# Performance work log

Hardware: AMD Instinct MI355X
Metric: run time of the kernel (lower is better)

## Reference

```python
import jax, jax.numpy as jnp
import numpy as np

N = 50000   # nodes
E = 800000  # edges (avg degree 16)
H = 8       # num_heads
D = 16      # head_dim = hidden_size // num_heads = 128 // 8


def setup_inputs() -> dict:
    key = jax.random.key(0)
    k1, k2, k3, k4, k5 = jax.random.split(key, 5)
    q = jax.random.normal(k1, (N, D, H), dtype=jnp.float32)
    k = jax.random.normal(k2, (N, D, H), dtype=jnp.float32)
    v = jax.random.normal(k3, (N, D, H), dtype=jnp.float32)
    # COO adjacency: row = destination node of each edge, col = source node
    row = jnp.sort(jax.random.randint(k4, (E,), 0, N, dtype=jnp.int32))
    col = jax.random.randint(k5, (E,), 0, N, dtype=jnp.int32)
    return {"q": q, "k": k, "v": v, "row": row, "col": col}


def reference(q, k, v, row, col):
    # bsddmm: sampled dense-dense matmul -> per-edge, per-head attention logits
    # logits[e, h] = sum_d q[row[e], d, h] * k[col[e], d, h]
    logits = jnp.einsum('edh,edh->eh', q[row], k[col])  # [E, H]

    # sparse softmax over each destination row (per head), numerically stable
    m = jax.ops.segment_max(logits, row, num_segments=N)  # [N, H]
    p = jnp.exp(logits - m[row])                          # [E, H]
    s = jax.ops.segment_sum(p, row, num_segments=N)       # [N, H]
    attn = p / s[row]                                     # [E, H]

    # bspmm: out[i, d, h] = sum_{e: row[e]==i} attn[e, h] * v[col[e], d, h]
    out = jax.ops.segment_sum(attn[:, None, :] * v[col], row, num_segments=N)  # [N, D, H]
    return out.reshape(N, -1)  # [N, D*H]
```

## Files before the change

kernel.cpp:

```cpp
#include <hip/hip_runtime.h>
#include <math.h>

#define HEADS 8
#define DIM 16
#define NPB 32

static __device__ __forceinline__ unsigned short f2bf(float f) {
  unsigned u = __float_as_uint(f);
  u += 0x7FFFu + ((u >> 16) & 1u);
  return (unsigned short)(u >> 16);
}
static __device__ __forceinline__ float bflo(unsigned u) { return __uint_as_float(u << 16); }
static __device__ __forceinline__ float bfhi(unsigned u) { return __uint_as_float(u & 0xFFFF0000u); }

__global__ __launch_bounds__(256) void conv_kernel(
    const float* __restrict__ k, const float* __restrict__ v,
    unsigned short* __restrict__ kv, int N) {
  int j = blockIdx.x * blockDim.x + threadIdx.x;
  if (j >= N * 32) return;
  int i = j >> 5, c = j & 31;
  const float* src = (c < 16 ? k : v) + (size_t)i * 128 + (c & 15) * 8;
  float4 f0 = ((const float4*)src)[0];
  float4 f1 = ((const float4*)src)[1];
  uint4 r;
  r.x = (unsigned)f2bf(f0.x) | ((unsigned)f2bf(f0.y) << 16);
  r.y = (unsigned)f2bf(f0.z) | ((unsigned)f2bf(f0.w) << 16);
  r.z = (unsigned)f2bf(f1.x) | ((unsigned)f2bf(f1.y) << 16);
  r.w = (unsigned)f2bf(f1.z) | ((unsigned)f2bf(f1.w) << 16);
  *(uint4*)(kv + (size_t)i * 256 + c * 8) = r;
}

__global__ __launch_bounds__(256) void spmha_bf16_kernel(
    const float* __restrict__ q, const unsigned short* __restrict__ kv,
    const int* __restrict__ row, const int* __restrict__ col,
    float* __restrict__ out, int N, int E) {
  __shared__ int rp[NPB + 1];
  int node0 = blockIdx.x * NPB;
  if (threadIdx.x <= NPB) {
    int target = node0 + threadIdx.x;
    int lo = 0, hi = E;
    while (lo < hi) {
      int mid = (lo + hi) >> 1;
      if (row[mid] < target) lo = mid + 1; else hi = mid;
    }
    rp[threadIdx.x] = lo;
  }
  __syncthreads();

  int il = threadIdx.x >> 3;
  int i  = node0 + il;
  int l  = threadIdx.x & 7;
  bool alive = (i < N);
  int s = alive ? rp[il] : 0;
  int e = alive ? rp[il + 1] : 0;

  float qv0[8], qv1[8];
  if (alive) {
    const float4* qp = (const float4*)(q + (size_t)i * 128);
    *(float4*)&qv0[0] = qp[2 * l];
    *(float4*)&qv0[4] = qp[2 * l + 1];
    *(float4*)&qv1[0] = qp[16 + 2 * l];
    *(float4*)&qv1[4] = qp[16 + 2 * l + 1];
  }

  float o0[8], o1[8], m[8], den[8];
#pragma unroll
  for (int h = 0; h < 8; ++h) { o0[h] = 0.f; o1[h] = 0.f; m[h] = -INFINITY; den[h] = 0.f; }

  auto cvt8 = [](const uint4& A, float* f) {
    f[0] = bflo(A.x); f[1] = bfhi(A.x); f[2] = bflo(A.y); f[3] = bfhi(A.y);
    f[4] = bflo(A.z); f[5] = bfhi(A.z); f[6] = bflo(A.w); f[7] = bfhi(A.w);
  };

  auto do_edge = [&](const uint4& A, const uint4& B, const uint4& C, const uint4& D) {
    float kf0[8], kf1[8], vf0[8], vf1[8];
    cvt8(A, kf0); cvt8(B, kf1); cvt8(C, vf0); cvt8(D, vf1);
    float part[8];
#pragma unroll
    for (int h = 0; h < 8; ++h) part[h] = fmaf(qv0[h], kf0[h], qv1[h] * kf1[h]);
#pragma unroll
    for (int h = 0; h < 8; ++h) part[h] += __shfl_xor(part[h], 1);
#pragma unroll
    for (int h = 0; h < 8; ++h) part[h] += __shfl_xor(part[h], 2);
#pragma unroll
    for (int h = 0; h < 8; ++h) part[h] += __shfl_xor(part[h], 4);
#pragma unroll
    for (int h = 0; h < 8; ++h) {
      float mn = fmaxf(m[h], part[h]);
      float sc = __expf(m[h] - mn);
      float p  = __expf(part[h] - mn);
      den[h] = fmaf(den[h], sc, p);
      m[h] = mn;
      o0[h] = fmaf(o0[h], sc, p * vf0[h]);
      o1[h] = fmaf(o1[h], sc, p * vf1[h]);
    }
  };

  int eidx = s;
  for (; eidx + 2 <= e; eidx += 2) {
    int c0 = col[eidx];
    int c1 = col[eidx + 1];
    const uint4* b0 = (const uint4*)(kv + (size_t)c0 * 256);
    const uint4* b1 = (const uint4*)(kv + (size_t)c1 * 256);
    uint4 A0 = b0[l], B0 = b0[8 + l], C0 = b0[16 + l], D0 = b0[24 + l];
    uint4 A1 = b1[l], B1 = b1[8 + l], C1 = b1[16 + l], D1 = b1[24 + l];
    do_edge(A0, B0, C0, D0);
    do_edge(A1, B1, C1, D1);
  }
  if (eidx < e) {
    int c0 = col[eidx];
    const uint4* b0 = (const uint4*)(kv + (size_t)c0 * 256);
    do_edge(b0[l], b0[8 + l], b0[16 + l], b0[24 + l]);
  }

  if (alive) {
    float inv[8];
#pragma unroll
    for (int h = 0; h < 8; ++h) inv[h] = (e > s) ? 1.f / den[h] : 0.f;
    float4* op = (float4*)(out + (size_t)i * 128);
    float4 r;
    r.x = o0[0] * inv[0]; r.y = o0[1] * inv[1]; r.z = o0[2] * inv[2]; r.w = o0[3] * inv[3];
    op[2 * l] = r;
    r.x = o0[4] * inv[4]; r.y = o0[5] * inv[5]; r.z = o0[6] * inv[6]; r.w = o0[7] * inv[7];
    op[2 * l + 1] = r;
    r.x = o1[0] * inv[0]; r.y = o1[1] * inv[1]; r.z = o1[2] * inv[2]; r.w = o1[3] * inv[3];
    op[16 + 2 * l] = r;
    r.x = o1[4] * inv[4]; r.y = o1[5] * inv[5]; r.z = o1[6] * inv[6]; r.w = o1[7] * inv[7];
    op[16 + 2 * l + 1] = r;
  }
}

__global__ __launch_bounds__(256) void spmha_f32_kernel(
    const float* __restrict__ q, const float* __restrict__ k, const float* __restrict__ v,
    const int* __restrict__ row, const int* __restrict__ col,
    float* __restrict__ out, int N, int E) {
  __shared__ int rp[NPB + 1];
  int node0 = blockIdx.x * NPB;
  if (threadIdx.x <= NPB) {
    int target = node0 + threadIdx.x;
    int lo = 0, hi = E;
    while (lo < hi) {
      int mid = (lo + hi) >> 1;
      if (row[mid] < target) lo = mid + 1; else hi = mid;
    }
    rp[threadIdx.x] = lo;
  }
  __syncthreads();

  int il = threadIdx.x >> 3;
  int i  = node0 + il;
  int l  = threadIdx.x & 7;
  bool alive = (i < N);
  int s = alive ? rp[il] : 0;
  int e = alive ? rp[il + 1] : 0;

  float qv[16];
  if (alive) {
    const float4* qb = (const float4*)(q + (size_t)i * 128);
#pragma unroll
    for (int r = 0; r < 4; ++r) *(float4*)&qv[4 * r] = qb[8 * r + l];
  }
  float o[16];
#pragma unroll
  for (int x = 0; x < 16; ++x) o[x] = 0.f;
  float m[4], den[4];
#pragma unroll
  for (int j = 0; j < 4; ++j) { m[j] = -INFINITY; den[j] = 0.f; }

  auto do_edge = [&](const float* kk, const float* vv) {
    float part[4];
#pragma unroll
    for (int j = 0; j < 4; ++j) part[j] = 0.f;
#pragma unroll
    for (int r = 0; r < 4; ++r)
#pragma unroll
      for (int j = 0; j < 4; ++j)
        part[j] = fmaf(qv[4 * r + j], kk[4 * r + j], part[j]);
#pragma unroll
    for (int j = 0; j < 4; ++j) {
      part[j] += __shfl_xor(part[j], 2);
      part[j] += __shfl_xor(part[j], 4);
    }
#pragma unroll
    for (int j = 0; j < 4; ++j) {
      float mn = fmaxf(m[j], part[j]);
      float sc = __expf(m[j] - mn);
      float p  = __expf(part[j] - mn);
      den[j] = fmaf(den[j], sc, p);
      m[j] = mn;
#pragma unroll
      for (int r = 0; r < 4; ++r)
        o[4 * r + j] = fmaf(o[4 * r + j], sc, p * vv[4 * r + j]);
    }
  };

  int eidx = s;
  for (; eidx < e; ++eidx) {
    int c0 = col[eidx];
    const float4* kb0 = (const float4*)(k + (size_t)c0 * 128);
    const float4* vb0 = (const float4*)(v + (size_t)c0 * 128);
    float kk0[16], vv0[16];
#pragma unroll
    for (int r = 0; r < 4; ++r) {
      *(float4*)&kk0[4 * r] = kb0[8 * r + l];
      *(float4*)&vv0[4 * r] = vb0[8 * r + l];
    }
    do_edge(kk0, vv0);
  }

  if (alive) {
    float inv[4];
#pragma unroll
    for (int j = 0; j < 4; ++j) inv[j] = (e > s) ? 1.f / den[j] : 0.f;
    float4* ob = (float4*)(out + (size_t)i * 128);
#pragma unroll
    for (int r = 0; r < 4; ++r) {
      float4 res;
      res.x = o[4 * r + 0] * inv[0];
      res.y = o[4 * r + 1] * inv[1];
      res.z = o[4 * r + 2] * inv[2];
      res.w = o[4 * r + 3] * inv[3];
      ob[8 * r + l] = res;
    }
  }
}

extern "C" void kernel_launch(void* const* d_in, const int* in_sizes, int n_in,
                              void* d_out, int out_size, void* d_ws, size_t ws_size,
                              hipStream_t stream) {
  const float* q   = (const float*)d_in[0];
  const float* k   = (const float*)d_in[1];
  const float* v   = (const float*)d_in[2];
  const int*   row = (const int*)d_in[3];
  const int*   col = (const int*)d_in[4];
  float* out = (float*)d_out;

  int N = in_sizes[0] / (DIM * HEADS);
  int E = in_sizes[3];

  size_t kv_bytes = (size_t)N * 512;
  int total = N * HEADS;
  int grid = (total + 255) / 256;

  if (ws_size >= kv_bytes) {
    unsigned short* kv = (unsigned short*)d_ws;
    int cgrid = (N * 32 + 255) / 256;
    conv_kernel<<<cgrid, 256, 0, stream>>>(k, v, kv, N);
    spmha_bf16_kernel<<<grid, 256, 0, stream>>>(q, kv, row, col, out, N, E);
  } else {
    spmha_f32_kernel<<<grid, 256, 0, stream>>>(q, k, v, row, col, out, N, E);
  }
}
```

Baseline: 239.8 us.

## Split each node's edge list across two thread groups and merge softmax states

The bf16 kernel now assigns two 8-lane groups per destination node, each handling alternating edges (stride 4 with two-edge unroll), so each block covers 16 nodes instead of 32. The partial online-softmax states (max, denominator, accumulators) are combined with a cross-lane shuffle and only one group writes the output. The aim is more parallelism per node and more memory-level parallelism for the gathers, which shortens per-thread serial edge chains. The cost is twice as many blocks, repeated binary searches, and extra shuffle and exp work in the merge.

New measurement: 218.6 us. 1.1x faster.

```diff
diff --git a/kernel.cpp b/kernel.cpp
--- a/kernel.cpp
+++ b/kernel.cpp
@@ -3,7 +3,7 @@
 
 #define HEADS 8
 #define DIM 16
-#define NPB 32
+#define NPB 16
 
 static __device__ __forceinline__ unsigned short f2bf(float f) {
   unsigned u = __float_as_uint(f);
@@ -47,7 +47,9 @@
   }
   __syncthreads();
 
-  int il = threadIdx.x >> 3;
+  int g  = threadIdx.x >> 3;
+  int il = g >> 1;
+  int sl = g & 1;
   int i  = node0 + il;
   int l  = threadIdx.x & 7;
   bool alive = (i < N);
@@ -96,10 +98,10 @@
     }
   };
 
-  int eidx = s;
-  for (; eidx + 2 <= e; eidx += 2) {
+  int eidx = s + sl;
+  for (; eidx + 2 < e; eidx += 4) {
     int c0 = col[eidx];
-    int c1 = col[eidx + 1];
+    int c1 = col[eidx + 2];
     const uint4* b0 = (const uint4*)(kv + (size_t)c0 * 256);
     const uint4* b1 = (const uint4*)(kv + (size_t)c1 * 256);
     uint4 A0 = b0[l], B0 = b0[8 + l], C0 = b0[16 + l], D0 = b0[24 + l];
@@ -113,20 +115,39 @@
     do_edge(b0[l], b0[8 + l], b0[16 + l], b0[24 + l]);
   }
 
-  if (alive) {
-    float inv[8];
-#pragma unroll
-    for (int h = 0; h < 8; ++h) inv[h] = (e > s) ? 1.f / den[h] : 0.f;
+#pragma unroll
+  for (int h = 0; h < 8; ++h) {
+    float m_o   = __shfl_xor(m[h], 8);
+    float den_o = __shfl_xor(den[h], 8);
+    float o0_o  = __shfl_xor(o0[h], 8);
+    float o1_o  = __shfl_xor(o1[h], 8);
+    float mn = fmaxf(m[h], m_o);
+    float a  = __expf(m[h] - mn);
+    float b  = __expf(m_o - mn);
+    den[h] = den[h] * a + den_o * b;
+    o0[h]  = o0[h] * a + o0_o * b;
+    o1[h]  = o1[h] * a + o1_o * b;
+  }
+
+  if (alive && sl == 0) {
     float4* op = (float4*)(out + (size_t)i * 128);
-    float4 r;
-    r.x = o0[0] * inv[0]; r.y = o0[1] * inv[1]; r.z = o0[2] * inv[2]; r.w = o0[3] * inv[3];
-    op[2 * l] = r;
-    r.x = o0[4] * inv[4]; r.y = o0[5] * inv[5]; r.z = o0[6] * inv[6]; r.w = o0[7] * inv[7];
-    op[2 * l + 1] = r;
-    r.x = o1[0] * inv[0]; r.y = o1[1] * inv[1]; r.z = o1[2] * inv[2]; r.w = o1[3] * inv[3];
-    op[16 + 2 * l] = r;
-    r.x = o1[4] * inv[4]; r.y = o1[5] * inv[5]; r.z = o1[6] * inv[6]; r.w = o1[7] * inv[7];
-    op[16 + 2 * l + 1] = r;
+    if (e > s) {
+      float inv[8];
+#pragma unroll
+      for (int h = 0; h < 8; ++h) inv[h] = 1.f / den[h];
+      float4 r;
+      r.x = o0[0] * inv[0]; r.y = o0[1] * inv[1]; r.z = o0[2] * inv[2]; r.w = o0[3] * inv[3];
+      op[2 * l] = r;
+      r.x = o0[4] * inv[4]; r.y = o0[5] * inv[5]; r.z = o0[6] * inv[6]; r.w = o0[7] * inv[7];
+      op[2 * l + 1] = r;
+      r.x = o1[0] * inv[0]; r.y = o1[1] * inv[1]; r.z = o1[2] * inv[2]; r.w = o1[3] * inv[3];
+      op[16 + 2 * l] = r;
+      r.x = o1[4] * inv[4]; r.y = o1[5] * inv[5]; r.z = o1[6] * inv[6]; r.w = o1[7] * inv[7];
+      op[16 + 2 * l + 1] = r;
+    } else {
+      float4 z = make_float4(0.f, 0.f, 0.f, 0.f);
+      op[2 * l] = z; op[2 * l + 1] = z; op[16 + 2 * l] = z; op[16 + 2 * l + 1] = z;
+    }
   }
 }
 
@@ -134,9 +155,9 @@
     const float* __restrict__ q, const float* __restrict__ k, const float* __restrict__ v,
     const int* __restrict__ row, const int* __restrict__ col,
     float* __restrict__ out, int N, int E) {
-  __shared__ int rp[NPB + 1];
-  int node0 = blockIdx.x * NPB;
-  if (threadIdx.x <= NPB) {
+  __shared__ int rp[33];
+  int node0 = blockIdx.x * 32;
+  if (threadIdx.x <= 32) {
     int target = node0 + threadIdx.x;
     int lo = 0, hi = E;
     while (lo < hi) {
@@ -194,8 +215,7 @@
     }
   };
 
-  int eidx = s;
-  for (; eidx < e; ++eidx) {
+  for (int eidx = s; eidx < e; ++eidx) {
     int c0 = col[eidx];
     const float4* kb0 = (const float4*)(k + (size_t)c0 * 128);
     const float4* vb0 = (const float4*)(v + (size_t)c0 * 128);
@@ -239,15 +259,16 @@
   int E = in_sizes[3];
 
   size_t kv_bytes = (size_t)N * 512;
-  int total = N * HEADS;
-  int grid = (total + 255) / 256;
 
   if (ws_size >= kv_bytes) {
     unsigned short* kv = (unsigned short*)d_ws;
     int cgrid = (N * 32 + 255) / 256;
     conv_kernel<<<cgrid, 256, 0, stream>>>(k, v, kv, N);
+    int grid = (N + NPB - 1) / NPB;
     spmha_bf16_kernel<<<grid, 256, 0, stream>>>(q, kv, row, col, out, N, E);
   } else {
+    int total = N * HEADS;
+    int grid = (total + 255) / 256;
     spmha_f32_kernel<<<grid, 256, 0, stream>>>(q, k, v, row, col, out, N, E);
   }
 }
```
